# Optimization experiments

Hardware: AMD Instinct MI355X
Metric: run time of the kernel (lower is better)

The kernel has to match this reference:

```python
import jax, jax.numpy as jnp
import numpy as np

NUM_NODES = 200000
EMB_DIM = 64
NUM_EDGES = 6400000
NUM_LAYERS = 4


def setup_inputs() -> dict:
    key = jax.random.key(0)
    k1, k2, k3, k4 = jax.random.split(key, 4)
    embeds = jax.random.normal(k1, (NUM_NODES, EMB_DIM), dtype=jnp.float32)
    adj_rows = jax.random.randint(k2, (NUM_EDGES,), 0, NUM_NODES, dtype=jnp.int64)
    adj_cols = jax.random.randint(k3, (NUM_EDGES,), 0, NUM_NODES, dtype=jnp.int64)
    adj_vals = jax.random.uniform(k4, (NUM_EDGES,), dtype=jnp.float32)
    return {"embeds": embeds, "adj_rows": adj_rows, "adj_cols": adj_cols, "adj_vals": adj_vals}


def _spmm(rows, cols, vals, x):
    # Sparse (COO) adjacency @ dense x: out[r] += v * x[c]
    msgs = vals[:, None] * x[cols]  # [E, d] gather + scale
    return jax.ops.segment_sum(msgs, rows, num_segments=NUM_NODES)


def reference(embeds, adj_rows, adj_cols, adj_vals):
    x = embeds
    acc = x  # running sum over layer outputs (fuses stack+mean)
    for _ in range(NUM_LAYERS):
        x = _spmm(adj_rows, adj_cols, adj_vals, x)
        acc = acc + x
    return acc / jnp.float32(NUM_LAYERS + 1)
```

## Files before the change

kernel.cpp:

```cpp
#include <hip/hip_runtime.h>

#define N_NODES 200000
#define DIM 64
#define BSHIFT 9
#define NB 391
#define NB_PAD 512
#define CHUNK 4096

__device__ __forceinline__ float bf2f(unsigned short u) {
    return __uint_as_float(((unsigned int)u) << 16);
}
__device__ __forceinline__ unsigned short f2bf(float f) {
    unsigned int u = __float_as_uint(f);
    u += 0x7FFFu + ((u >> 16) & 1u);
    return (unsigned short)(u >> 16);
}

__global__ __launch_bounds__(256) void bucket_hist(const int* __restrict__ rows, int E,
                                                   int* __restrict__ bcnt) {
    __shared__ int h[NB_PAD];
    for (int i = threadIdx.x; i < NB_PAD; i += 256) h[i] = 0;
    __syncthreads();
    int stride = gridDim.x * blockDim.x;
    for (int e = blockIdx.x * blockDim.x + threadIdx.x; e < E; e += stride)
        atomicAdd(&h[rows[e] >> BSHIFT], 1);
    __syncthreads();
    for (int i = threadIdx.x; i < NB; i += 256)
        if (h[i]) atomicAdd(&bcnt[i], h[i]);
}

__global__ void bucket_scan(const int* __restrict__ bcnt, int* __restrict__ bbase,
                            int* __restrict__ bcur) {
    if (threadIdx.x == 0 && blockIdx.x == 0) {
        int run = 0;
        for (int i = 0; i < NB; i++) { bbase[i] = run; bcur[i] = run; run += bcnt[i]; }
        bbase[NB] = run;
    }
}

__global__ __launch_bounds__(256) void bucket_scatter(const int* __restrict__ rows,
                                                      const int* __restrict__ cols,
                                                      const float* __restrict__ vals, int E,
                                                      int* __restrict__ bcur,
                                                      int2* __restrict__ tmp) {
    __shared__ int h[NB_PAD];
    __shared__ int incl[NB_PAD];
    __shared__ int sbuf[NB_PAD];
    __shared__ int fix[NB_PAD];
    __shared__ int cur2[NB_PAD];
    __shared__ int2 stage[CHUNK];
    __shared__ unsigned short sbkt[CHUNK];
    const int base = blockIdx.x * CHUNK;
    const int count = min(CHUNK, E - base);
    const int t = threadIdx.x;

    for (int i = t; i < NB_PAD; i += 256) h[i] = 0;
    __syncthreads();
    for (int i = t; i < count; i += 256)
        atomicAdd(&h[rows[base + i] >> BSHIFT], 1);
    __syncthreads();
    for (int i = t; i < NB_PAD; i += 256) incl[i] = h[i];
    __syncthreads();
    for (int off = 1; off < NB_PAD; off <<= 1) {
        for (int i = t; i < NB_PAD; i += 256)
            sbuf[i] = incl[i] + ((i >= off) ? incl[i - off] : 0);
        __syncthreads();
        for (int i = t; i < NB_PAD; i += 256) incl[i] = sbuf[i];
        __syncthreads();
    }
    for (int i = t; i < NB; i += 256) {
        int excl = incl[i] - h[i];
        int g = h[i] ? atomicAdd(&bcur[i], h[i]) : 0;
        fix[i] = g - excl;
        cur2[i] = excl;
    }
    __syncthreads();
    for (int i = t; i < count; i += 256) {
        int r = rows[base + i];
        int b = r >> BSHIFT;
        int slot = atomicAdd(&cur2[b], 1);
        int key = ((r & ((1 << BSHIFT) - 1)) << 18) | cols[base + i];
        stage[slot] = make_int2(key, __float_as_int(vals[base + i]));
        sbkt[slot] = (unsigned short)b;
    }
    __syncthreads();
    for (int s = t; s < count; s += 256)
        tmp[s + fix[sbkt[s]]] = stage[s];
}

__global__ __launch_bounds__(256) void bucket_sort(const int2* __restrict__ tmp,
                                                   const int* __restrict__ bbase,
                                                   int2* __restrict__ sorted,
                                                   int* __restrict__ row_start) {
    __shared__ int h[NB_PAD];
    __shared__ int sums[256];
    const int b = blockIdx.x;
    const int s0 = bbase[b], s1 = bbase[b + 1];
    const int t = threadIdx.x;
    h[t] = 0; h[t + 256] = 0;
    __syncthreads();
    for (int e = s0 + t; e < s1; e += 256)
        atomicAdd(&h[tmp[e].x >> 18], 1);
    __syncthreads();
    int a0 = h[2 * t], a1 = h[2 * t + 1];
    sums[t] = a0 + a1;
    __syncthreads();
    if (t == 0) {
        int run = 0;
        for (int i = 0; i < 256; i++) { int v = sums[i]; sums[i] = run; run += v; }
    }
    __syncthreads();
    int e0 = sums[t];
    h[2 * t] = e0;
    h[2 * t + 1] = e0 + a0;
    __syncthreads();
    int rbase = b << BSHIFT;
    for (int r = t; r < (1 << BSHIFT); r += 256) {
        int row = rbase + r;
        if (row < N_NODES) row_start[row] = s0 + h[r];
    }
    if (b == NB - 1 && t == 0) row_start[N_NODES] = s1;
    __syncthreads();
    for (int e = s0 + t; e < s1; e += 256) {
        int2 kv = tmp[e];
        int r = kv.x >> 18;
        int rank = atomicAdd(&h[r], 1);
        sorted[s0 + rank] = make_int2(kv.x & 0x3FFFF, kv.y);
    }
}

__global__ __launch_bounds__(256) void convert_kernel(const float* __restrict__ src,
                                                      unsigned short* __restrict__ dst, int n4) {
    int i = blockIdx.x * blockDim.x + threadIdx.x;
    if (i >= n4) return;
    float4 v = *(const float4*)(src + i * 4);
    ushort4 o;
    o.x = f2bf(v.x); o.y = f2bf(v.y); o.z = f2bf(v.z); o.w = f2bf(v.w);
    *(ushort4*)(dst + i * 4) = o;
}

template <int MODE>
__global__ __launch_bounds__(256) void spmm_kernel(const int2* __restrict__ sorted,
                                                   const int* __restrict__ row_start,
                                                   const unsigned short* __restrict__ xb,
                                                   const float* __restrict__ embeds,
                                                   unsigned short* __restrict__ y,
                                                   float* __restrict__ acc) {
    int gid = blockIdx.x * blockDim.x + threadIdx.x;
    int r = gid >> 4;
    if (r >= N_NODES) return;
    int j = (gid & 15) << 2;
    int e = row_start[r], eend = row_start[r + 1];
    float4 a = make_float4(0.f, 0.f, 0.f, 0.f);
    for (; e + 4 <= eend; e += 4) {
        int2 c0 = sorted[e];
        int2 c1 = sorted[e + 1];
        int2 c2 = sorted[e + 2];
        int2 c3 = sorted[e + 3];
        ushort4 u0 = *(const ushort4*)(xb + (c0.x << 6) + j);
        ushort4 u1 = *(const ushort4*)(xb + (c1.x << 6) + j);
        ushort4 u2 = *(const ushort4*)(xb + (c2.x << 6) + j);
        ushort4 u3 = *(const ushort4*)(xb + (c3.x << 6) + j);
        float v0 = __int_as_float(c0.y), v1 = __int_as_float(c1.y);
        float v2 = __int_as_float(c2.y), v3 = __int_as_float(c3.y);
        a.x = fmaf(v0, bf2f(u0.x), a.x); a.y = fmaf(v0, bf2f(u0.y), a.y);
        a.z = fmaf(v0, bf2f(u0.z), a.z); a.w = fmaf(v0, bf2f(u0.w), a.w);
        a.x = fmaf(v1, bf2f(u1.x), a.x); a.y = fmaf(v1, bf2f(u1.y), a.y);
        a.z = fmaf(v1, bf2f(u1.z), a.z); a.w = fmaf(v1, bf2f(u1.w), a.w);
        a.x = fmaf(v2, bf2f(u2.x), a.x); a.y = fmaf(v2, bf2f(u2.y), a.y);
        a.z = fmaf(v2, bf2f(u2.z), a.z); a.w = fmaf(v2, bf2f(u2.w), a.w);
        a.x = fmaf(v3, bf2f(u3.x), a.x); a.y = fmaf(v3, bf2f(u3.y), a.y);
        a.z = fmaf(v3, bf2f(u3.z), a.z); a.w = fmaf(v3, bf2f(u3.w), a.w);
    }
    for (; e < eend; ++e) {
        int2 cv = sorted[e];
        ushort4 u = *(const ushort4*)(xb + (cv.x << 6) + j);
        float v = __int_as_float(cv.y);
        a.x = fmaf(v, bf2f(u.x), a.x);
        a.y = fmaf(v, bf2f(u.y), a.y);
        a.z = fmaf(v, bf2f(u.z), a.z);
        a.w = fmaf(v, bf2f(u.w), a.w);
    }
    int o = (r << 6) + j;
    if (MODE == 0) {
        ushort4 yo; yo.x = f2bf(a.x); yo.y = f2bf(a.y); yo.z = f2bf(a.z); yo.w = f2bf(a.w);
        *(ushort4*)(y + o) = yo;
        const float4 x0 = *(const float4*)(embeds + o);
        *(float4*)(acc + o) = make_float4(x0.x + a.x, x0.y + a.y, x0.z + a.z, x0.w + a.w);
    } else if (MODE == 1) {
        ushort4 yo; yo.x = f2bf(a.x); yo.y = f2bf(a.y); yo.z = f2bf(a.z); yo.w = f2bf(a.w);
        *(ushort4*)(y + o) = yo;
        float4 c = *(const float4*)(acc + o);
        *(float4*)(acc + o) = make_float4(c.x + a.x, c.y + a.y, c.z + a.z, c.w + a.w);
    } else {
        float4 c = *(const float4*)(acc + o);
        const float s = 0.2f;
        *(float4*)(acc + o) = make_float4((c.x + a.x) * s, (c.y + a.y) * s,
                                          (c.z + a.z) * s, (c.w + a.w) * s);
    }
}

extern "C" void kernel_launch(void* const* d_in, const int* in_sizes, int n_in,
                              void* d_out, int out_size, void* d_ws, size_t ws_size,
                              hipStream_t stream) {
    const float* embeds = (const float*)d_in[0];
    const int*   rows   = (const int*)d_in[1];
    const int*   cols   = (const int*)d_in[2];
    const float* vals   = (const float*)d_in[3];
    float* acc = (float*)d_out;
    const int E = in_sizes[1];

    char* ws = (char*)d_ws;
    size_t off = 0;
    auto alloc = [&](size_t bytes) -> char* {
        char* p = ws + off;
        off = (off + bytes + 255) & ~(size_t)255;
        return p;
    };
    int*   bcnt      = (int*)alloc((size_t)NB * 4);
    int*   bbase     = (int*)alloc((size_t)(NB + 1) * 4);
    int*   bcur      = (int*)alloc((size_t)NB * 4);
    int*   row_start = (int*)alloc((size_t)(N_NODES + 1) * 4);
    int2*  sorted    = (int2*)alloc((size_t)E * 8);
    unsigned short* xb0 = (unsigned short*)alloc((size_t)N_NODES * DIM * 2);
    unsigned short* xb1 = (unsigned short*)alloc((size_t)N_NODES * DIM * 2);
    int2*  tmp       = (int2*)alloc((size_t)E * 8);

    hipMemsetAsync(bcnt, 0, (size_t)NB * 4, stream);

    bucket_hist<<<512, 256, 0, stream>>>(rows, E, bcnt);
    bucket_scan<<<1, 64, 0, stream>>>(bcnt, bbase, bcur);
    bucket_scatter<<<(E + CHUNK - 1) / CHUNK, 256, 0, stream>>>(rows, cols, vals, E, bcur, tmp);
    bucket_sort<<<NB, 256, 0, stream>>>(tmp, bbase, sorted, row_start);

    int n4 = N_NODES * DIM / 4;
    convert_kernel<<<(n4 + 255) / 256, 256, 0, stream>>>(embeds, xb0, n4);

    int sb = (N_NODES * 16 + 255) / 256;
    spmm_kernel<0><<<sb, 256, 0, stream>>>(sorted, row_start, xb0, embeds, xb1, acc);
    spmm_kernel<1><<<sb, 256, 0, stream>>>(sorted, row_start, xb1, embeds, xb0, acc);
    spmm_kernel<1><<<sb, 256, 0, stream>>>(sorted, row_start, xb0, embeds, xb1, acc);
    spmm_kernel<2><<<sb, 256, 0, stream>>>(sorted, row_start, xb1, embeds, xb0, acc);
}
```

Measured before the change: 882.7 us.

## Rework bucket sort scans, halve bucket size, widen SpMM gathers with prefetch

The bucket size drops from 512 to 256 rows, giving 782 buckets. The serial single-thread scans in bucket_scan and bucket_sort are replaced by wavefront shuffle scans, and bucket_scatter now holds each edge in registers so rows are read only once. The SpMM kernel uses 8 threads per row with 16-byte bf16 gathers and software-prefetches the next four edge entries, which is meant to cut per-edge instruction and latency overhead. The trade-offs are higher register pressure and fewer threads per row, so less memory parallelism per row.

```diff
diff --git a/kernel.cpp b/kernel.cpp
--- a/kernel.cpp
+++ b/kernel.cpp
@@ -2,9 +2,10 @@
 
 #define N_NODES 200000
 #define DIM 64
-#define BSHIFT 9
-#define NB 391
-#define NB_PAD 512
+#define BSHIFT 8
+#define BROWS 256
+#define NB 782
+#define NB_PAD 1024
 #define CHUNK 4096
 
 __device__ __forceinline__ float bf2f(unsigned short u) {
@@ -29,99 +30,144 @@
         if (h[i]) atomicAdd(&bcnt[i], h[i]);
 }
 
-__global__ void bucket_scan(const int* __restrict__ bcnt, int* __restrict__ bbase,
-                            int* __restrict__ bcur) {
-    if (threadIdx.x == 0 && blockIdx.x == 0) {
-        int run = 0;
-        for (int i = 0; i < NB; i++) { bbase[i] = run; bcur[i] = run; run += bcnt[i]; }
-        bbase[NB] = run;
-    }
-}
-
-__global__ __launch_bounds__(256) void bucket_scatter(const int* __restrict__ rows,
+__global__ __launch_bounds__(1024) void bucket_scan(const int* __restrict__ bcnt,
+                                                    int* __restrict__ bbase,
+                                                    int* __restrict__ bcur) {
+    __shared__ int wsum[16];
+    int t = threadIdx.x;
+    int v = (t < NB) ? bcnt[t] : 0;
+    int incl = v;
+    for (int off = 1; off < 64; off <<= 1) {
+        int u = __shfl_up(incl, off);
+        if ((t & 63) >= off) incl += u;
+    }
+    if ((t & 63) == 63) wsum[t >> 6] = incl;
+    __syncthreads();
+    if (t < 16) {
+        int w = wsum[t];
+        for (int off = 1; off < 16; off <<= 1) {
+            int u = __shfl_up(w, off);
+            if (t >= off) w += u;
+        }
+        wsum[t] = w;
+    }
+    __syncthreads();
+    int wb = (t >= 64) ? wsum[(t >> 6) - 1] : 0;
+    int excl = wb + incl - v;
+    if (t < NB) { bbase[t] = excl; bcur[t] = excl; }
+    if (t == NB - 1) bbase[NB] = excl + v;
+}
+
+__global__ __launch_bounds__(512) void bucket_scatter(const int* __restrict__ rows,
                                                       const int* __restrict__ cols,
                                                       const float* __restrict__ vals, int E,
                                                       int* __restrict__ bcur,
                                                       int2* __restrict__ tmp) {
     __shared__ int h[NB_PAD];
-    __shared__ int incl[NB_PAD];
-    __shared__ int sbuf[NB_PAD];
-    __shared__ int fix[NB_PAD];
     __shared__ int cur2[NB_PAD];
+    __shared__ int wtot[8];
     __shared__ int2 stage[CHUNK];
     __shared__ unsigned short sbkt[CHUNK];
     const int base = blockIdx.x * CHUNK;
     const int count = min(CHUNK, E - base);
     const int t = threadIdx.x;
 
-    for (int i = t; i < NB_PAD; i += 256) h[i] = 0;
-    __syncthreads();
-    for (int i = t; i < count; i += 256)
-        atomicAdd(&h[rows[base + i] >> BSHIFT], 1);
-    __syncthreads();
-    for (int i = t; i < NB_PAD; i += 256) incl[i] = h[i];
-    __syncthreads();
-    for (int off = 1; off < NB_PAD; off <<= 1) {
-        for (int i = t; i < NB_PAD; i += 256)
-            sbuf[i] = incl[i] + ((i >= off) ? incl[i - off] : 0);
-        __syncthreads();
-        for (int i = t; i < NB_PAD; i += 256) incl[i] = sbuf[i];
-        __syncthreads();
-    }
-    for (int i = t; i < NB; i += 256) {
-        int excl = incl[i] - h[i];
-        int g = h[i] ? atomicAdd(&bcur[i], h[i]) : 0;
-        fix[i] = g - excl;
-        cur2[i] = excl;
-    }
-    __syncthreads();
-    for (int i = t; i < count; i += 256) {
-        int r = rows[base + i];
-        int b = r >> BSHIFT;
-        int slot = atomicAdd(&cur2[b], 1);
-        int key = ((r & ((1 << BSHIFT) - 1)) << 18) | cols[base + i];
-        stage[slot] = make_int2(key, __float_as_int(vals[base + i]));
-        sbkt[slot] = (unsigned short)b;
-    }
-    __syncthreads();
-    for (int s = t; s < count; s += 256)
-        tmp[s + fix[sbkt[s]]] = stage[s];
-}
-
-__global__ __launch_bounds__(256) void bucket_sort(const int2* __restrict__ tmp,
+    for (int i = t; i < NB_PAD; i += 512) h[i] = 0;
+    __syncthreads();
+
+    int myr[8], myc[8];
+    float myv[8];
+#pragma unroll
+    for (int k = 0; k < 8; ++k) {
+        int i = t + k * 512;
+        if (i < count) {
+            myr[k] = rows[base + i];
+            myc[k] = cols[base + i];
+            myv[k] = vals[base + i];
+            atomicAdd(&h[myr[k] >> BSHIFT], 1);
+        }
+    }
+    __syncthreads();
+
+    int h0 = h[2 * t], h1 = h[2 * t + 1];
+    int s = h0 + h1;
+    int incl = s;
+    for (int off = 1; off < 64; off <<= 1) {
+        int u = __shfl_up(incl, off);
+        if ((t & 63) >= off) incl += u;
+    }
+    if ((t & 63) == 63) wtot[t >> 6] = incl;
+    __syncthreads();
+    int wb = 0;
+    for (int w = 0; w < (t >> 6); ++w) wb += wtot[w];
+    int excl = wb + incl - s;
+    cur2[2 * t] = excl;
+    cur2[2 * t + 1] = excl + h0;
+    __syncthreads();
+
+    for (int i = t; i < NB; i += 512) {
+        int hi = h[i];
+        int g = hi ? atomicAdd(&bcur[i], hi) : 0;
+        h[i] = g - cur2[i];
+    }
+    __syncthreads();
+
+#pragma unroll
+    for (int k = 0; k < 8; ++k) {
+        int i = t + k * 512;
+        if (i < count) {
+            int r = myr[k];
+            int b = r >> BSHIFT;
+            int slot = atomicAdd(&cur2[b], 1);
+            stage[slot] = make_int2(((r & (BROWS - 1)) << 18) | myc[k], __float_as_int(myv[k]));
+            sbkt[slot] = (unsigned short)b;
+        }
+    }
+    __syncthreads();
+    for (int s2 = t; s2 < count; s2 += 512)
+        tmp[s2 + h[sbkt[s2]]] = stage[s2];
+}
+
+__global__ __launch_bounds__(512) void bucket_sort(const int2* __restrict__ tmp,
                                                    const int* __restrict__ bbase,
                                                    int2* __restrict__ sorted,
                                                    int* __restrict__ row_start) {
-    __shared__ int h[NB_PAD];
-    __shared__ int sums[256];
+    __shared__ int h[BROWS];
+    __shared__ int hbase[BROWS];
+    __shared__ int wtot[4];
     const int b = blockIdx.x;
     const int s0 = bbase[b], s1 = bbase[b + 1];
     const int t = threadIdx.x;
-    h[t] = 0; h[t + 256] = 0;
-    __syncthreads();
-    for (int e = s0 + t; e < s1; e += 256)
+    if (t < BROWS) h[t] = 0;
+    __syncthreads();
+    for (int e = s0 + t; e < s1; e += 512)
         atomicAdd(&h[tmp[e].x >> 18], 1);
     __syncthreads();
-    int a0 = h[2 * t], a1 = h[2 * t + 1];
-    sums[t] = a0 + a1;
-    __syncthreads();
-    if (t == 0) {
-        int run = 0;
-        for (int i = 0; i < 256; i++) { int v = sums[i]; sums[i] = run; run += v; }
-    }
-    __syncthreads();
-    int e0 = sums[t];
-    h[2 * t] = e0;
-    h[2 * t + 1] = e0 + a0;
-    __syncthreads();
-    int rbase = b << BSHIFT;
-    for (int r = t; r < (1 << BSHIFT); r += 256) {
-        int row = rbase + r;
-        if (row < N_NODES) row_start[row] = s0 + h[r];
+    int v = 0, incl = 0;
+    if (t < BROWS) {
+        v = h[t];
+        incl = v;
+        for (int off = 1; off < 64; off <<= 1) {
+            int u = __shfl_up(incl, off);
+            if ((t & 63) >= off) incl += u;
+        }
+        if ((t & 63) == 63) wtot[t >> 6] = incl;
+    }
+    __syncthreads();
+    if (t < BROWS) {
+        int wb = 0;
+        for (int w = 0; w < (t >> 6); ++w) wb += wtot[w];
+        hbase[t] = wb + incl - v;
+    }
+    __syncthreads();
+    if (t < BROWS) {
+        h[t] = hbase[t];
+        int row = (b << BSHIFT) + t;
+        if (row < N_NODES) row_start[row] = s0 + hbase[t];
     }
     if (b == NB - 1 && t == 0) row_start[N_NODES] = s1;
     __syncthreads();
-    for (int e = s0 + t; e < s1; e += 256) {
+    for (int e = s0 + t; e < s1; e += 512) {
         int2 kv = tmp[e];
         int r = kv.x >> 18;
         int rank = atomicAdd(&h[r], 1);
@@ -139,6 +185,20 @@
     *(ushort4*)(dst + i * 4) = o;
 }
 
+#define BF_LO(u) __uint_as_float((u) << 16)
+#define BF_HI(u) __uint_as_float((u) & 0xFFFF0000u)
+#define FMA8(G, V)                              \
+    do {                                        \
+        a0 = fmaf((V), BF_LO((G).x), a0);       \
+        a1 = fmaf((V), BF_HI((G).x), a1);       \
+        a2 = fmaf((V), BF_LO((G).y), a2);       \
+        a3 = fmaf((V), BF_HI((G).y), a3);       \
+        a4 = fmaf((V), BF_LO((G).z), a4);       \
+        a5 = fmaf((V), BF_HI((G).z), a5);       \
+        a6 = fmaf((V), BF_LO((G).w), a6);       \
+        a7 = fmaf((V), BF_HI((G).w), a7);       \
+    } while (0)
+
 template <int MODE>
 __global__ __launch_bounds__(256) void spmm_kernel(const int2* __restrict__ sorted,
                                                    const int* __restrict__ row_start,
@@ -147,56 +207,79 @@
                                                    unsigned short* __restrict__ y,
                                                    float* __restrict__ acc) {
     int gid = blockIdx.x * blockDim.x + threadIdx.x;
-    int r = gid >> 4;
+    int r = gid >> 3;
     if (r >= N_NODES) return;
-    int j = (gid & 15) << 2;
+    int j = (gid & 7) << 3;
+    const unsigned short* xbj = xb + j;
     int e = row_start[r], eend = row_start[r + 1];
-    float4 a = make_float4(0.f, 0.f, 0.f, 0.f);
-    for (; e + 4 <= eend; e += 4) {
-        int2 c0 = sorted[e];
-        int2 c1 = sorted[e + 1];
-        int2 c2 = sorted[e + 2];
-        int2 c3 = sorted[e + 3];
-        ushort4 u0 = *(const ushort4*)(xb + (c0.x << 6) + j);
-        ushort4 u1 = *(const ushort4*)(xb + (c1.x << 6) + j);
-        ushort4 u2 = *(const ushort4*)(xb + (c2.x << 6) + j);
-        ushort4 u3 = *(const ushort4*)(xb + (c3.x << 6) + j);
+    float a0 = 0.f, a1 = 0.f, a2 = 0.f, a3 = 0.f, a4 = 0.f, a5 = 0.f, a6 = 0.f, a7 = 0.f;
+
+    int2 c0 = make_int2(0, 0), c1 = make_int2(0, 0);
+    int2 c2 = make_int2(0, 0), c3 = make_int2(0, 0);
+    if (e + 4 <= eend) {
+        c0 = sorted[e]; c1 = sorted[e + 1]; c2 = sorted[e + 2]; c3 = sorted[e + 3];
+    }
+    while (e + 8 <= eend) {
+        uint4 g0 = *(const uint4*)(xbj + (c0.x << 6));
+        uint4 g1 = *(const uint4*)(xbj + (c1.x << 6));
+        uint4 g2 = *(const uint4*)(xbj + (c2.x << 6));
+        uint4 g3 = *(const uint4*)(xbj + (c3.x << 6));
+        int2 n0 = sorted[e + 4], n1 = sorted[e + 5];
+        int2 n2 = sorted[e + 6], n3 = sorted[e + 7];
         float v0 = __int_as_float(c0.y), v1 = __int_as_float(c1.y);
         float v2 = __int_as_float(c2.y), v3 = __int_as_float(c3.y);
-        a.x = fmaf(v0, bf2f(u0.x), a.x); a.y = fmaf(v0, bf2f(u0.y), a.y);
-        a.z = fmaf(v0, bf2f(u0.z), a.z); a.w = fmaf(v0, bf2f(u0.w), a.w);
-        a.x = fmaf(v1, bf2f(u1.x), a.x); a.y = fmaf(v1, bf2f(u1.y), a.y);
-        a.z = fmaf(v1, bf2f(u1.z), a.z); a.w = fmaf(v1, bf2f(u1.w), a.w);
-        a.x = fmaf(v2, bf2f(u2.x), a.x); a.y = fmaf(v2, bf2f(u2.y), a.y);
-        a.z = fmaf(v2, bf2f(u2.z), a.z); a.w = fmaf(v2, bf2f(u2.w), a.w);
-        a.x = fmaf(v3, bf2f(u3.x), a.x); a.y = fmaf(v3, bf2f(u3.y), a.y);
-        a.z = fmaf(v3, bf2f(u3.z), a.z); a.w = fmaf(v3, bf2f(u3.w), a.w);
+        FMA8(g0, v0); FMA8(g1, v1); FMA8(g2, v2); FMA8(g3, v3);
+        c0 = n0; c1 = n1; c2 = n2; c3 = n3;
+        e += 4;
+    }
+    if (e + 4 <= eend) {
+        uint4 g0 = *(const uint4*)(xbj + (c0.x << 6));
+        uint4 g1 = *(const uint4*)(xbj + (c1.x << 6));
+        uint4 g2 = *(const uint4*)(xbj + (c2.x << 6));
+        uint4 g3 = *(const uint4*)(xbj + (c3.x << 6));
+        float v0 = __int_as_float(c0.y), v1 = __int_as_float(c1.y);
+        float v2 = __int_as_float(c2.y), v3 = __int_as_float(c3.y);
+        FMA8(g0, v0); FMA8(g1, v1); FMA8(g2, v2); FMA8(g3, v3);
+        e += 4;
     }
     for (; e < eend; ++e) {
         int2 cv = sorted[e];
-        ushort4 u = *(const ushort4*)(xb + (cv.x << 6) + j);
+        uint4 g = *(const uint4*)(xbj + (cv.x << 6));
         float v = __int_as_float(cv.y);
-        a.x = fmaf(v, bf2f(u.x), a.x);
-        a.y = fmaf(v, bf2f(u.y), a.y);
-        a.z = fmaf(v, bf2f(u.z), a.z);
-        a.w = fmaf(v, bf2f(u.w), a.w);
-    }
+        FMA8(g, v);
+    }
+
     int o = (r << 6) + j;
     if (MODE == 0) {
-        ushort4 yo; yo.x = f2bf(a.x); yo.y = f2bf(a.y); yo.z = f2bf(a.z); yo.w = f2bf(a.w);
-        *(ushort4*)(y + o) = yo;
-        const float4 x0 = *(const float4*)(embeds + o);
-        *(float4*)(acc + o) = make_float4(x0.x + a.x, x0.y + a.y, x0.z + a.z, x0.w + a.w);
+        uint4 yo;
+        yo.x = (unsigned)f2bf(a0) | ((unsigned)f2bf(a1) << 16);
+        yo.y = (unsigned)f2bf(a2) | ((unsigned)f2bf(a3) << 16);
+        yo.z = (unsigned)f2bf(a4) | ((unsigned)f2bf(a5) << 16);
+        yo.w = (unsigned)f2bf(a6) | ((unsigned)f2bf(a7) << 16);
+        *(uint4*)(y + o) = yo;
+        float4 x0 = *(const float4*)(embeds + o);
+        float4 x1 = *(const float4*)(embeds + o + 4);
+        *(float4*)(acc + o)     = make_float4(x0.x + a0, x0.y + a1, x0.z + a2, x0.w + a3);
+        *(float4*)(acc + o + 4) = make_float4(x1.x + a4, x1.y + a5, x1.z + a6, x1.w + a7);
     } else if (MODE == 1) {
-        ushort4 yo; yo.x = f2bf(a.x); yo.y = f2bf(a.y); yo.z = f2bf(a.z); yo.w = f2bf(a.w);
-        *(ushort4*)(y + o) = yo;
-        float4 c = *(const float4*)(acc + o);
-        *(float4*)(acc + o) = make_float4(c.x + a.x, c.y + a.y, c.z + a.z, c.w + a.w);
+        uint4 yo;
+        yo.x = (unsigned)f2bf(a0) | ((unsigned)f2bf(a1) << 16);
+        yo.y = (unsigned)f2bf(a2) | ((unsigned)f2bf(a3) << 16);
+        yo.z = (unsigned)f2bf(a4) | ((unsigned)f2bf(a5) << 16);
+        yo.w = (unsigned)f2bf(a6) | ((unsigned)f2bf(a7) << 16);
+        *(uint4*)(y + o) = yo;
+        float4 q0 = *(const float4*)(acc + o);
+        float4 q1 = *(const float4*)(acc + o + 4);
+        *(float4*)(acc + o)     = make_float4(q0.x + a0, q0.y + a1, q0.z + a2, q0.w + a3);
+        *(float4*)(acc + o + 4) = make_float4(q1.x + a4, q1.y + a5, q1.z + a6, q1.w + a7);
     } else {
-        float4 c = *(const float4*)(acc + o);
-        const float s = 0.2f;
-        *(float4*)(acc + o) = make_float4((c.x + a.x) * s, (c.y + a.y) * s,
-                                          (c.z + a.z) * s, (c.w + a.w) * s);
+        const float sc = 0.2f;
+        float4 q0 = *(const float4*)(acc + o);
+        float4 q1 = *(const float4*)(acc + o + 4);
+        *(float4*)(acc + o)     = make_float4((q0.x + a0) * sc, (q0.y + a1) * sc,
+                                              (q0.z + a2) * sc, (q0.w + a3) * sc);
+        *(float4*)(acc + o + 4) = make_float4((q1.x + a4) * sc, (q1.y + a5) * sc,
+                                              (q1.z + a6) * sc, (q1.w + a7) * sc);
     }
 }
 
@@ -228,15 +311,15 @@
 
     hipMemsetAsync(bcnt, 0, (size_t)NB * 4, stream);
 
-    bucket_hist<<<512, 256, 0, stream>>>(rows, E, bcnt);
-    bucket_scan<<<1, 64, 0, stream>>>(bcnt, bbase, bcur);
-    bucket_scatter<<<(E + CHUNK - 1) / CHUNK, 256, 0, stream>>>(rows, cols, vals, E, bcur, tmp);
-    bucket_sort<<<NB, 256, 0, stream>>>(tmp, bbase, sorted, row_start);
+    bucket_hist<<<1024, 256, 0, stream>>>(rows, E, bcnt);
+    bucket_scan<<<1, 1024, 0, stream>>>(bcnt, bbase, bcur);
+    bucket_scatter<<<(E + CHUNK - 1) / CHUNK, 512, 0, stream>>>(rows, cols, vals, E, bcur, tmp);
+    bucket_sort<<<NB, 512, 0, stream>>>(tmp, bbase, sorted, row_start);
 
     int n4 = N_NODES * DIM / 4;
     convert_kernel<<<(n4 + 255) / 256, 256, 0, stream>>>(embeds, xb0, n4);
 
-    int sb = (N_NODES * 16 + 255) / 256;
+    int sb = (N_NODES * 8 + 255) / 256;
     spmm_kernel<0><<<sb, 256, 0, stream>>>(sorted, row_start, xb0, embeds, xb1, acc);
     spmm_kernel<1><<<sb, 256, 0, stream>>>(sorted, row_start, xb1, embeds, xb0, acc);
     spmm_kernel<1><<<sb, 256, 0, stream>>>(sorted, row_start, xb0, embeds, xb1, acc);
```

New measurement: 823.2 us. 1.07x faster.
